# Kernel tuning notes

Measured on AMD Instinct MI355X. Metric: run time of the kernel, lower is better.

The kernel has to match this reference:

```python
import jax, jax.numpy as jnp
import numpy as np

D_MODEL = 1024
NUM_HEADS = 16
D_KEY = 64
CTX = 2048
B, T = 2, 2048


def setup_inputs() -> dict:
    key = jax.random.key(0)
    ks = jax.random.split(key, 5)
    scale_in = 1.0 / np.sqrt(D_MODEL)
    scale_out = 1.0 / np.sqrt(NUM_HEADS * D_KEY)
    return {
        "X": jax.random.normal(ks[0], (B, T, D_MODEL), dtype=jnp.float32),
        "Wqkv": jax.random.uniform(ks[1], (D_MODEL, 3 * NUM_HEADS * D_KEY), dtype=jnp.float32, minval=-scale_in, maxval=scale_in),
        "bqkv": jax.random.uniform(ks[2], (3 * NUM_HEADS * D_KEY,), dtype=jnp.float32, minval=-scale_in, maxval=scale_in),
        "Wout": jax.random.uniform(ks[3], (NUM_HEADS * D_KEY, D_MODEL), dtype=jnp.float32, minval=-scale_out, maxval=scale_out),
        "bout": jax.random.uniform(ks[4], (D_MODEL,), dtype=jnp.float32, minval=-scale_out, maxval=scale_out),
    }


def reference(X, Wqkv, bqkv, Wout, bout):
    b, t, _ = X.shape
    # project and split into q, k, v: [B,T,3,H,Dk]
    qkv = (X @ Wqkv + bqkv).reshape(b, t, 3, NUM_HEADS, D_KEY)
    q = qkv[:, :, 0].transpose(0, 2, 1, 3)  # [B,H,T,Dk]
    k = qkv[:, :, 1].transpose(0, 2, 1, 3)
    v = qkv[:, :, 2].transpose(0, 2, 1, 3)
    scores = jnp.einsum("bhqd,bhkd->bhqk", q, k) / jnp.sqrt(jnp.float32(D_KEY))
    causal = jnp.tril(jnp.ones((t, t), dtype=bool))  # [T,T]
    scores = jnp.where(causal, scores, -jnp.inf)
    attn = jax.nn.softmax(scores, axis=-1)
    out = jnp.einsum("bhqk,bhkd->bhqd", attn, v)  # [B,H,T,Dk]
    out = out.transpose(0, 2, 1, 3).reshape(b, t, NUM_HEADS * D_KEY)
    return out @ Wout + bout
```

## Files before the change

### kernel.cpp

```cpp
#include <hip/hip_runtime.h>
#include <hip/hip_bf16.h>
#include <math.h>

static constexpr int Bc = 2, Hc = 16, Tc = 2048, DKc = 64, DMc = 1024, NQKV = 3072;
#define QSCALE 0.18033688011112042f

typedef unsigned short u16;
typedef unsigned int u32;
typedef short s8v __attribute__((ext_vector_type(8)));
typedef float f32x4 __attribute__((ext_vector_type(4)));
typedef float f32x16 __attribute__((ext_vector_type(16)));
typedef int i32x4 __attribute__((ext_vector_type(4)));

#define DEVINL __device__ __forceinline__

DEVINL u16 f2b(float f) {
    union { float f; unsigned u; } v; v.f = f;
    unsigned u = v.u;
    unsigned r = (u + 0x7fffu + ((u >> 16) & 1u)) >> 16;
    return (u16)r;
}

DEVINL u32 pkbf16(float lo, float up) {
    u32 r;
    asm volatile("v_cvt_pk_bf16_f32 %0, %1, %2" : "=v"(r) : "v"(lo), "v"(up));
    return r;
}

DEVINL float vexp2(float x) {
    float r;
    asm("v_exp_f32 %0, %1" : "=v"(r) : "v"(x));
    return r;
}

DEVINL void pl32swap(u32& a, u32& b) {
    asm volatile("v_permlane32_swap_b32 %0, %1" : "+v"(a), "+v"(b));
}

DEVINL void gl_lds(const void* g, void* l) {
    __builtin_amdgcn_global_load_lds(
        (const __attribute__((address_space(1))) unsigned int*)g,
        (__attribute__((address_space(3))) unsigned int*)l, 16, 0, 0);
}

DEVINL s8v as_s8v(i32x4 x) { union { i32x4 i; s8v v; } u; u.i = x; return u.v; }

__global__ __launch_bounds__(256) void conv_bf16(const float* __restrict__ in,
                                                 u16* __restrict__ outp, int n4) {
    int i = blockIdx.x * 256 + threadIdx.x;
    const int stride = gridDim.x * 256;
    for (; i < n4; i += stride) {
        float4 f = ((const float4*)in)[i];
        union { u16 u[4]; uint2 d; } o;
        o.u[0] = f2b(f.x); o.u[1] = f2b(f.y); o.u[2] = f2b(f.z); o.u[3] = f2b(f.w);
        ((uint2*)outp)[i] = o.d;
    }
}

__global__ __launch_bounds__(256) void transw(const float* __restrict__ W,
                                              u16* __restrict__ Wt, int N, int K) {
    __shared__ u16 LT[64][72];
    const int n0 = blockIdx.x * 64, k0 = blockIdx.y * 64;
    const int t = threadIdx.x;
    const int rr = t >> 4, cc = (t & 15) * 4;
    #pragma unroll
    for (int it = 0; it < 4; it++) {
        const int row = it * 16 + rr;
        float4 f = *(const float4*)&W[(size_t)(k0 + row) * N + n0 + cc];
        union { u16 u[4]; uint2 d; } o;
        o.u[0] = f2b(f.x); o.u[1] = f2b(f.y); o.u[2] = f2b(f.z); o.u[3] = f2b(f.w);
        *(uint2*)&LT[row][cc] = o.d;
    }
    __syncthreads();
    #pragma unroll
    for (int it = 0; it < 4; it++) {
        const int nrow = it * 16 + rr;
        union { u16 u[4]; uint2 d; } o;
        #pragma unroll
        for (int j = 0; j < 4; j++) o.u[j] = LT[cc + j][nrow];
        *(uint2*)&Wt[(size_t)(n0 + nrow) * K + k0 + cc] = o.d;
    }
}

template <int EPI>
__global__ __launch_bounds__(512) void gemm_8w(
    const u16* __restrict__ A, const u16* __restrict__ Bt,
    const float* __restrict__ bias,
    u16* __restrict__ q_out, u16* __restrict__ k_out, u16* __restrict__ v_out,
    float* __restrict__ f_out, int M, int N, int K, int ntn)
{
    __shared__ __align__(16) u16 Al[2][128 * 32];
    __shared__ __align__(16) u16 Bl[2][128 * 32];
    const int tid = threadIdx.x, lane = tid & 63, w = tid >> 6;
    const int qd = gridDim.x >> 3;
    const int wg = (blockIdx.x & 7) * qd + (blockIdx.x >> 3);
    const int m0 = (wg / ntn) * 128, n0 = (wg % ntn) * 128;
    const int wm = w >> 2, wn = w & 3;

    f32x4 acc[4][2] = {};
    const int nt = K >> 5;

    const int srow = tid >> 2;
    const int skc  = ((tid & 3) ^ ((srow >> 1) & 3)) * 8;

#define STG(t_, s_) do {                                                       \
        const int kk_ = (t_) << 5;                                             \
        gl_lds(A + (size_t)(m0 + srow) * K + kk_ + skc,                        \
               (char*)&Al[s_][0] + w * 1024);                                  \
        gl_lds(Bt + (size_t)(n0 + srow) * K + kk_ + skc,                       \
               (char*)&Bl[s_][0] + w * 1024);                                  \
    } while (0)

    STG(0, 0);
    __syncthreads();
    int buf = 0;
    for (int t = 0; t < nt; t++) {
        if (t + 1 < nt) STG(t + 1, buf ^ 1);
        s8v af[4], bf[2];
        #pragma unroll
        for (int mi = 0; mi < 4; mi++) {
            const int row = wm * 64 + mi * 16 + (lane & 15);
            const int slot = (lane >> 4) ^ ((row >> 1) & 3);
            af[mi] = *(const s8v*)((const char*)&Al[buf][0] + row * 64 + slot * 16);
        }
        #pragma unroll
        for (int ni = 0; ni < 2; ni++) {
            const int row = wn * 32 + ni * 16 + (lane & 15);
            const int slot = (lane >> 4) ^ ((row >> 1) & 3);
            bf[ni] = *(const s8v*)((const char*)&Bl[buf][0] + row * 64 + slot * 16);
        }
        #pragma unroll
        for (int mi = 0; mi < 4; mi++)
            #pragma unroll
            for (int ni = 0; ni < 2; ni++)
                acc[mi][ni] = __builtin_amdgcn_mfma_f32_16x16x32_bf16(af[mi], bf[ni], acc[mi][ni], 0, 0, 0);
        __syncthreads();
        buf ^= 1;
    }
#undef STG

    #pragma unroll
    for (int mi = 0; mi < 4; mi++)
    #pragma unroll
    for (int ni = 0; ni < 2; ni++)
    #pragma unroll
    for (int r = 0; r < 4; r++) {
        const int row = m0 + wm * 64 + mi * 16 + (lane >> 4) * 4 + r;
        const int col = n0 + wn * 32 + ni * 16 + (lane & 15);
        const float val = acc[mi][ni][r] + bias[col];
        if constexpr (EPI == 0) {
            const int sel = col >> 10, rem = col & 1023;
            const int h = rem >> 6, d = rem & 63;
            const int b = row >> 11, tt = row & 2047;
            const size_t idx = ((size_t)(b * Hc + h) * Tc + tt) * DKc + d;
            if (sel == 0) q_out[idx] = f2b(val * QSCALE);
            else if (sel == 1) k_out[idx] = f2b(val);
            else v_out[idx] = f2b(val);
        } else {
            f_out[(size_t)row * N + col] = val;
        }
    }
}

__global__ __launch_bounds__(512) void attn_fwd(
    const u16* __restrict__ Q, const u16* __restrict__ K,
    const u16* __restrict__ V, u16* __restrict__ O)
{
    __shared__ __align__(16) char Gl[2][2][2][8192];

    const int bid = blockIdx.x;
    const int bh = bid & 31;
    const int qt = 15 - (bid >> 5);
    const int tid = threadIdx.x;
    const int g = tid >> 8;
    const int gtid = tid & 255;
    const int lane = tid & 63;
    const int ws = (tid >> 6) & 3;
    const int hi = lane >> 5, lq = lane & 31;
    const int q0w = qt * 128 + ws * 32;
    const int qg = q0w + lq;

    const u16* Qb = Q + (size_t)bh * (Tc * DKc);
    const u16* Kb = K + (size_t)bh * (Tc * DKc);
    const u16* Vb = V + (size_t)bh * (Tc * DKc);

    s8v qf[4];
    #pragma unroll
    for (int st = 0; st < 4; st++)
        qf[st] = *(const s8v*)(Qb + (size_t)qg * 64 + st * 16 + hi * 8);

    f32x16 o0 = {}, o1 = {}, lacc = {};

    const int dtw = (q0w + 31) >> 6;
    const int h = qt + 1;
    const int t0 = g * h;

    char* const Kbase = &Gl[g][0][0][0];
    char* const Vbase = &Gl[g][1][0][0];

    const int d2 = (gtid & 31) * 2, kb8 = gtid >> 5;
    const unsigned vsw0 = ((unsigned)(d2 & 7)) << 4;
    const unsigned vsw1 = ((unsigned)((d2 + 1) & 7)) << 4;
    const unsigned ksw = ((unsigned)(lq & 7)) << 4;

    u32 vx[8];

#define ISSUE_K(kt_, dst_) do {                                              \
        const char* Ktile_ = (const char*)(Kb + (size_t)(kt_) * 4096);       \
        _Pragma("unroll")                                                    \
        for (int s_ = 0; s_ < 2; s_++) {                                     \
            const int o_ = s_ * 4096 + gtid * 16;                            \
            const int rk_ = o_ >> 7;                                         \
            const int cb_ = (o_ & 127) ^ ((rk_ & 7) << 4);                   \
            gl_lds(Ktile_ + rk_ * 128 + cb_, (dst_) + s_ * 4096 + ws * 1024); \
        }                                                                    \
    } while (0)

#define LOAD_V(kt_) do {                                                     \
        const u16* Vtile_ = Vb + (size_t)(kt_) * 4096;                       \
        _Pragma("unroll")                                                    \
        for (int i_ = 0; i_ < 8; i_++)                                       \
            vx[i_] = *(const u32*)(Vtile_ + (kb8 * 8 + i_) * 64 + d2);       \
    } while (0)

#define WRITE_V(dst_) do {                                                   \
        s8v v0_, v1_;                                                        \
        _Pragma("unroll")                                                    \
        for (int i_ = 0; i_ < 8; i_++) {                                     \
            v0_[i_] = (short)(vx[i_] & 0xffff);                              \
            v1_[i_] = (short)(vx[i_] >> 16);                                 \
        }                                                                    \
        *(s8v*)((dst_) + d2 * 128 + (((unsigned)(kb8 * 16)) ^ vsw0)) = v0_;  \
        *(s8v*)((dst_) + (d2 + 1) * 128 + (((unsigned)(kb8 * 16)) ^ vsw1)) = v1_; \
    } while (0)

    ISSUE_K(t0, Kbase);
    LOAD_V(t0);
    WRITE_V(Vbase);
    __syncthreads();

    int c = 0;
    for (int i = 0; i < h; i++) {
        const int tki = t0 + i;
        const bool pf_next = (i + 1 < h);
        if (pf_next) {
            ISSUE_K(tki + 1, Kbase + (c ^ 1) * 8192);
            LOAD_V(tki + 1);
        }

        if (tki <= dtw) {
            const char* Kc = Kbase + c * 8192;
            const char* Vc = Vbase + c * 8192;
            f32x16 s0v = {}, s1v = {};
            __builtin_amdgcn_s_setprio(1);
            #pragma unroll
            for (int st = 0; st < 4; st++) {
                const unsigned cbs = (unsigned)(st * 32 + hi * 16);
                s8v kf0 = *(const s8v*)(Kc + lq * 128 + (cbs ^ ksw));
                s8v kf1 = *(const s8v*)(Kc + (32 + lq) * 128 + (cbs ^ ksw));
                s0v = __builtin_amdgcn_mfma_f32_32x32x16_bf16(kf0, qf[st], s0v, 0, 0, 0);
                s1v = __builtin_amdgcn_mfma_f32_32x32x16_bf16(kf1, qf[st], s1v, 0, 0, 0);
            }
            __builtin_amdgcn_s_setprio(0);

            if (tki == dtw) {
                #pragma unroll
                for (int r = 0; r < 16; r++) {
                    const int kg = tki * 64 + (r & 3) + 8 * (r >> 2) + 4 * hi;
                    if (kg > qg) s0v[r] = -INFINITY;
                    if (kg + 32 > qg) s1v[r] = -INFINITY;
                }
            }

            #pragma unroll
            for (int r = 0; r < 16; r++) {
                s0v[r] = vexp2(s0v[r]);
                s1v[r] = vexp2(s1v[r]);
            }
            lacc += s0v;
            lacc += s1v;

            i32x4 pf[4];
            #pragma unroll
            for (int gq = 0; gq < 2; gq++) {
                #pragma unroll
                for (int hq = 0; hq < 2; hq++) {
                    const int base = hq * 8;
                    u32 a0, a1, b0, b1;
                    if (gq == 0) {
                        a0 = pkbf16(s0v[base + 0], s0v[base + 1]);
                        a1 = pkbf16(s0v[base + 2], s0v[base + 3]);
                        b0 = pkbf16(s0v[base + 4], s0v[base + 5]);
                        b1 = pkbf16(s0v[base + 6], s0v[base + 7]);
                    } else {
                        a0 = pkbf16(s1v[base + 0], s1v[base + 1]);
                        a1 = pkbf16(s1v[base + 2], s1v[base + 3]);
                        b0 = pkbf16(s1v[base + 4], s1v[base + 5]);
                        b1 = pkbf16(s1v[base + 6], s1v[base + 7]);
                    }
                    pl32swap(a0, b0);
                    pl32swap(a1, b1);
                    pf[gq * 2 + hq][0] = (int)a0;
                    pf[gq * 2 + hq][1] = (int)a1;
                    pf[gq * 2 + hq][2] = (int)b0;
                    pf[gq * 2 + hq][3] = (int)b1;
                }
            }

            __builtin_amdgcn_s_setprio(1);
            #pragma unroll
            for (int ks = 0; ks < 4; ks++) {
                const unsigned cbv = (unsigned)(ks * 32 + hi * 16);
                s8v vf0 = *(const s8v*)(Vc + lq * 128 + (cbv ^ ksw));
                s8v vf1 = *(const s8v*)(Vc + (32 + lq) * 128 + (cbv ^ ksw));
                const s8v pa = as_s8v(pf[ks]);
                o0 = __builtin_amdgcn_mfma_f32_32x32x16_bf16(pa, vf0, o0, 0, 0, 0);
                o1 = __builtin_amdgcn_mfma_f32_32x32x16_bf16(pa, vf1, o1, 0, 0, 0);
            }
            __builtin_amdgcn_s_setprio(0);
        }

        if (pf_next) WRITE_V(Vbase + (c ^ 1) * 8192);
        __syncthreads();
        c ^= 1;
    }

    float t8[8];
    #pragma unroll
    for (int r = 0; r < 8; r++) t8[r] = lacc[r] + lacc[r + 8];
    #pragma unroll
    for (int off = 4; off >= 1; off >>= 1)
        #pragma unroll
        for (int r = 0; r < off; r++) t8[r] = t8[r] + t8[r + off];
    float ls = t8[0] + __shfl_xor(t8[0], 32);

    float* Pf = (float*)(&Gl[0][0][0][0]) + ws * 2304;
    if (g == 1) {
        float* dst = Pf + lane * 34;
        #pragma unroll
        for (int r = 0; r < 16; r++) { dst[r] = o0[r]; dst[16 + r] = o1[r]; }
        Pf[2176 + lane] = ls;
    }
    __syncthreads();
    if (g == 0) {
        const float* src = Pf + lane * 34;
        #pragma unroll
        for (int r = 0; r < 16; r++) { o0[r] += src[r]; o1[r] += src[16 + r]; }
        ls += Pf[2176 + lane];

        const float linv = 1.0f / ls;
        const int b = bh >> 4, hh = bh & 15;
        u16* Ob = O + ((size_t)b * Tc) * DMc + hh * 64;
        #pragma unroll
        for (int r = 0; r < 16; r++) {
            const int cr = (r & 3) + 8 * (r >> 2) + 4 * hi;
            const float ir = __shfl(linv, cr);
            u16* orow = Ob + (size_t)(q0w + cr) * DMc;
            orow[lq]      = f2b(o0[r] * ir);
            orow[32 + lq] = f2b(o1[r] * ir);
        }
    }
#undef ISSUE_K
#undef LOAD_V
#undef WRITE_V
}

extern "C" void kernel_launch(void* const* d_in, const int* in_sizes, int n_in,
                              void* d_out, int out_size, void* d_ws, size_t ws_size,
                              hipStream_t stream)
{
    const float* X    = (const float*)d_in[0];
    const float* Wqkv = (const float*)d_in[1];
    const float* bqkv = (const float*)d_in[2];
    const float* Wout = (const float*)d_in[3];
    const float* bout = (const float*)d_in[4];
    float* out = (float*)d_out;

    char* ws = (char*)d_ws;
    u16* Xb  = (u16*)(ws);
    u16* Ow  = (u16*)(ws);
    u16* Wt1 = (u16*)(ws + (8 << 20));
    u16* Wt2 = (u16*)(ws + (14 << 20));
    u16* Qw  = (u16*)(ws + (16 << 20));
    u16* Kw  = (u16*)(ws + (24 << 20));
    u16* Vw  = (u16*)(ws + (32 << 20));

    conv_bf16<<<2048, 256, 0, stream>>>(X, Xb, (Bc * Tc * DMc) / 4);
    transw<<<dim3(NQKV / 64, DMc / 64), 256, 0, stream>>>(Wqkv, Wt1, NQKV, DMc);
    transw<<<dim3(DMc / 64, DMc / 64), 256, 0, stream>>>(Wout, Wt2, DMc, DMc);

    gemm_8w<0><<<768, 512, 0, stream>>>(
        Xb, Wt1, bqkv, Qw, Kw, Vw, nullptr, Bc * Tc, NQKV, DMc, NQKV / 128);

    attn_fwd<<<512, 512, 0, stream>>>(Qw, Kw, Vw, Ow);

    gemm_8w<1><<<256, 512, 0, stream>>>(
        Ow, Wt2, bout, nullptr, nullptr, nullptr, out, Bc * Tc, DMc, DMc, DMc / 128);
}
```

Before: 105.1 us.

## Use 256x256 eight-phase pipelined GEMM for QKV projection

Adds a new GEMM kernel with 256x256 output tiles split into four 128x128 quadrants. It interleaves LDS fragment loads, global-to-LDS staging and MFMA across eight barrier-separated phases per two K-steps, and raises MFMA issue priority with setprio. This is meant to improve operand reuse and overlap memory with compute for the QKV projection. The trade-off is only 192 workgroups on a 256-CU device, which risks underusing the GPU, plus heavy register use from 64 accumulator vectors.

```diff
diff --git a/kernel.cpp b/kernel.cpp
--- a/kernel.cpp
+++ b/kernel.cpp
@@ -79,6 +79,158 @@
         #pragma unroll
         for (int j = 0; j < 4; j++) o.u[j] = LT[cc + j][nrow];
         *(uint2*)&Wt[(size_t)(n0 + nrow) * K + k0 + cc] = o.d;
+    }
+}
+
+template <int EPI>
+__global__ __launch_bounds__(512) void gemm_8ph(
+    const u16* __restrict__ A, const u16* __restrict__ Bt,
+    const float* __restrict__ bias,
+    u16* __restrict__ q_out, u16* __restrict__ k_out, u16* __restrict__ v_out,
+    float* __restrict__ f_out, int M, int N, int K, int ntn)
+{
+    __shared__ __align__(16) u16 Al[2][2][8192];
+    __shared__ __align__(16) u16 Bl[2][2][8192];
+    const int tid = threadIdx.x, lane = tid & 63, w = tid >> 6;
+    const int qd = gridDim.x >> 3;
+    const int wg = (blockIdx.x & 7) * qd + (blockIdx.x >> 3);
+    const int m0 = (wg / ntn) * 256, n0 = (wg % ntn) * 256;
+    const int wrm = w >> 2, wrn = w & 3;
+
+    f32x4 acc[2][2][4][2] = {};
+    s8v af[4][2];
+    s8v bf[2][2][2];
+
+    const int iters = K >> 7;
+
+#define STG_H(mat_, gbase_, t_, dst_) do {                                     \
+        _Pragma("unroll")                                                      \
+        for (int i_ = 0; i_ < 2; i_++) {                                       \
+            const int r_ = i_ * 64 + (tid >> 3);                               \
+            gl_lds((mat_) + (size_t)((gbase_) + r_) * K + (t_) * 64            \
+                       + (((tid & 7) ^ (r_ & 7)) * 8),                         \
+                   (char*)(dst_) + i_ * 8192 + w * 1024);                      \
+        }                                                                      \
+    } while (0)
+
+#define LD_AF(sl_, mh_) do {                                                   \
+        _Pragma("unroll")                                                      \
+        for (int mi_ = 0; mi_ < 4; mi_++)                                      \
+        _Pragma("unroll")                                                      \
+        for (int ks_ = 0; ks_ < 2; ks_++) {                                    \
+            const int row_ = wrm * 64 + mi_ * 16 + (lane & 15);                \
+            const int slot_ = (ks_ * 4 + (lane >> 4)) ^ (row_ & 7);            \
+            af[mi_][ks_] = *(const s8v*)((const char*)&Al[sl_][mh_][0]         \
+                                         + row_ * 128 + slot_ * 16);           \
+        }                                                                      \
+    } while (0)
+
+#define LD_BF(sl_, nh_) do {                                                   \
+        _Pragma("unroll")                                                      \
+        for (int ni_ = 0; ni_ < 2; ni_++)                                      \
+        _Pragma("unroll")                                                      \
+        for (int ks_ = 0; ks_ < 2; ks_++) {                                    \
+            const int row_ = wrn * 32 + ni_ * 16 + (lane & 15);                \
+            const int slot_ = (ks_ * 4 + (lane >> 4)) ^ (row_ & 7);            \
+            bf[nh_][ni_][ks_] = *(const s8v*)((const char*)&Bl[sl_][nh_][0]    \
+                                              + row_ * 128 + slot_ * 16);      \
+        }                                                                      \
+    } while (0)
+
+#define MM(mh_, nh_) do {                                                      \
+        __builtin_amdgcn_s_setprio(1);                                         \
+        _Pragma("unroll")                                                      \
+        for (int mi_ = 0; mi_ < 4; mi_++)                                      \
+        _Pragma("unroll")                                                      \
+        for (int ni_ = 0; ni_ < 2; ni_++)                                      \
+        _Pragma("unroll")                                                      \
+        for (int ks_ = 0; ks_ < 2; ks_++)                                      \
+            acc[mh_][nh_][mi_][ni_] = __builtin_amdgcn_mfma_f32_16x16x32_bf16( \
+                af[mi_][ks_], bf[nh_][ni_][ks_], acc[mh_][nh_][mi_][ni_], 0, 0, 0); \
+        __builtin_amdgcn_s_setprio(0);                                         \
+    } while (0)
+
+#define BARX() do { __builtin_amdgcn_sched_barrier(0);                         \
+        __builtin_amdgcn_s_barrier();                                          \
+        __builtin_amdgcn_sched_barrier(0); } while (0)
+#define VMC(n_) asm volatile("s_waitcnt vmcnt(" #n_ ")" ::: "memory")
+
+    STG_H(A,  m0,       0, &Al[0][0][0]);
+    STG_H(Bt, n0,       0, &Bl[0][0][0]);
+    STG_H(Bt, n0 + 128, 0, &Bl[0][1][0]);
+    STG_H(A,  m0 + 128, 0, &Al[0][1][0]);
+    STG_H(A,  m0,       1, &Al[1][0][0]);
+    STG_H(Bt, n0,       1, &Bl[1][0][0]);
+    VMC(4);
+    BARX();
+
+    for (int j = 0; j < iters; ++j) {
+        const bool more = (j + 1 < iters);
+        const int t1 = 2 * j + 1, t2 = 2 * j + 2, t3 = 2 * j + 3;
+        LD_AF(0, 0); LD_BF(0, 0);
+        STG_H(Bt, n0 + 128, t1, &Bl[1][1][0]);
+        MM(0, 0);
+        BARX();
+        LD_BF(0, 1);
+        STG_H(A, m0 + 128, t1, &Al[1][1][0]);
+        MM(0, 1);
+        BARX();
+        LD_AF(0, 1);
+        if (more) STG_H(A, m0, t2, &Al[0][0][0]);
+        MM(1, 0);
+        BARX();
+        if (more) STG_H(Bt, n0, t2, &Bl[0][0][0]);
+        MM(1, 1);
+        if (more) { VMC(4); } else { VMC(0); }
+        BARX();
+        LD_AF(1, 0); LD_BF(1, 0);
+        if (more) STG_H(Bt, n0 + 128, t2, &Bl[0][1][0]);
+        MM(0, 0);
+        BARX();
+        LD_BF(1, 1);
+        if (more) STG_H(A, m0 + 128, t2, &Al[0][1][0]);
+        MM(0, 1);
+        BARX();
+        LD_AF(1, 1);
+        if (more) STG_H(A, m0, t3, &Al[1][0][0]);
+        MM(1, 0);
+        BARX();
+        if (more) STG_H(Bt, n0, t3, &Bl[1][0][0]);
+        MM(1, 1);
+        if (more) { VMC(4); }
+        BARX();
+    }
+#undef STG_H
+#undef LD_AF
+#undef LD_BF
+#undef MM
+#undef BARX
+#undef VMC
+
+    #pragma unroll
+    for (int mh = 0; mh < 2; mh++)
+    #pragma unroll
+    for (int nh = 0; nh < 2; nh++)
+    #pragma unroll
+    for (int mi = 0; mi < 4; mi++)
+    #pragma unroll
+    for (int ni = 0; ni < 2; ni++)
+    #pragma unroll
+    for (int r = 0; r < 4; r++) {
+        const int row = m0 + mh * 128 + wrm * 64 + mi * 16 + (lane >> 4) * 4 + r;
+        const int col = n0 + nh * 128 + wrn * 32 + ni * 16 + (lane & 15);
+        const float val = acc[mh][nh][mi][ni][r] + bias[col];
+        if constexpr (EPI == 0) {
+            const int sel = col >> 10, rem = col & 1023;
+            const int h = rem >> 6, d = rem & 63;
+            const int b = row >> 11, tt = row & 2047;
+            const size_t idx = ((size_t)(b * Hc + h) * Tc + tt) * DKc + d;
+            if (sel == 0) q_out[idx] = f2b(val * QSCALE);
+            else if (sel == 1) k_out[idx] = f2b(val);
+            else v_out[idx] = f2b(val);
+        } else {
+            f_out[(size_t)row * N + col] = val;
+        }
     }
 }
 
@@ -389,8 +541,8 @@
     transw<<<dim3(NQKV / 64, DMc / 64), 256, 0, stream>>>(Wqkv, Wt1, NQKV, DMc);
     transw<<<dim3(DMc / 64, DMc / 64), 256, 0, stream>>>(Wout, Wt2, DMc, DMc);
 
-    gemm_8w<0><<<768, 512, 0, stream>>>(
-        Xb, Wt1, bqkv, Qw, Kw, Vw, nullptr, Bc * Tc, NQKV, DMc, NQKV / 128);
+    gemm_8ph<0><<<192, 512, 0, stream>>>(
+        Xb, Wt1, bqkv, Qw, Kw, Vw, nullptr, Bc * Tc, NQKV, DMc, NQKV / 256);
 
     attn_fwd<<<512, 512, 0, stream>>>(Qw, Kw, Vw, Ow);
 
```

After: 106.7 us. Within noise of the previous version (+1.4%).
